# Performance work log

Hardware: AMD Instinct MI355X
Metric: run time of the kernel (lower is better)

The kernel has to match this reference:

```python
import jax, jax.numpy as jnp
import numpy as np

TOP_N = 16

def pairwise_l2(q, c):
    # Euclidean distance via ||q||^2 + ||c||^2 - 2 q.c, matching torch.cdist(p=2)
    qn = jnp.sum(q * q, axis=-1, keepdims=True)        # [B,S,1]
    cn = jnp.sum(c * c, axis=-1)[:, None, :]           # [B,1,C]
    d2 = qn + cn - 2.0 * jnp.einsum('bsd,bcd->bsc', q, c)
    return jnp.sqrt(jnp.maximum(d2, 0.0))

def setup_inputs() -> dict:
    key = jax.random.key(0)
    k1, k2, k3, k4, k5 = jax.random.split(key, 5)
    B, S, C, K, D = 4, 1024, 4096, 64, 256
    return {
        'query_embeddings': jax.random.normal(k1, (B, S, D), jnp.float32),
        'context_embeddings': jax.random.normal(k2, (B, C, D), jnp.float32),
        'memory_embeddings': jax.random.normal(k3, (B, K, D), jnp.float32),
        'W': jax.random.normal(k4, (D, D), jnp.float32) / jnp.sqrt(jnp.float32(D)),
        'b': jax.random.normal(k5, (D,), jnp.float32) * 0.01,
    }

def reference(query_embeddings, context_embeddings, memory_embeddings, W, b):
    # latent_query_projection (nn.Linear): x @ W^T + b
    qp = jnp.einsum('bsd,ed->bse', query_embeddings, W) + b
    d_ctx = pairwise_l2(qp, context_embeddings)                       # [B,S,C]
    mem = memory_embeddings.reshape(memory_embeddings.shape[0], -1,
                                    memory_embeddings.shape[-1])
    d_mem = pairwise_l2(qp, mem)                                      # [B,S,K]
    distances = jnp.concatenate([d_ctx, d_mem], axis=-1)              # [B,S,C+K]
    neg_top, idx = jax.lax.top_k(-distances, TOP_N)                   # smallest distances
    return -neg_top, idx
```

## Files before the change

### kernel.cpp

```cpp
#include <hip/hip_runtime.h>
#include <hip/hip_bf16.h>
#include <cfloat>
#include <cmath>

#define B_ 4
#define S_ 1024
#define C_ 4096
#define K_ 64
#define D_ 256
#define NC 4160
#define TOPN 16
#define CAND2 64

typedef __attribute__((ext_vector_type(8))) short short8;
typedef __attribute__((ext_vector_type(4))) float f32x4;

__global__ __launch_bounds__(256) void proj64_kernel(
    const float* __restrict__ q, const float* __restrict__ W,
    const float* __restrict__ bias, double* __restrict__ qp64,
    __hip_bfloat16* __restrict__ qpb)
{
  __shared__ alignas(16) float As[64][36];
  __shared__ alignas(16) float Ws[64][36];
  const int tid = threadIdx.x;
  const int m0 = blockIdx.x * 64;
  const int n0 = blockIdx.y * 64;
  const int tx = tid & 15;
  const int ty = tid >> 4;
  const int lr = tid >> 3;
  const int lk = (tid & 7) * 4;
  double acc[4][4] = {};
  for (int k0 = 0; k0 < D_; k0 += 32) {
    __syncthreads();
    {
      float4 a0 = *(const float4*)&q[(size_t)(m0 + lr) * D_ + k0 + lk];
      float4 a1 = *(const float4*)&q[(size_t)(m0 + lr + 32) * D_ + k0 + lk];
      *(float4*)&As[lr][lk] = a0;
      *(float4*)&As[lr + 32][lk] = a1;
      float4 w0 = *(const float4*)&W[(size_t)(n0 + lr) * D_ + k0 + lk];
      float4 w1 = *(const float4*)&W[(size_t)(n0 + lr + 32) * D_ + k0 + lk];
      *(float4*)&Ws[lr][lk] = w0;
      *(float4*)&Ws[lr + 32][lk] = w1;
    }
    __syncthreads();
    #pragma unroll
    for (int kk = 0; kk < 32; kk += 4) {
      float4 av[4], wv[4];
      #pragma unroll
      for (int i = 0; i < 4; ++i) av[i] = *(const float4*)&As[ty * 4 + i][kk];
      #pragma unroll
      for (int j = 0; j < 4; ++j) wv[j] = *(const float4*)&Ws[tx + 16 * j][kk];
      #pragma unroll
      for (int i = 0; i < 4; ++i)
        #pragma unroll
        for (int j = 0; j < 4; ++j) {
          acc[i][j] = fma((double)av[i].x, (double)wv[j].x, acc[i][j]);
          acc[i][j] = fma((double)av[i].y, (double)wv[j].y, acc[i][j]);
          acc[i][j] = fma((double)av[i].z, (double)wv[j].z, acc[i][j]);
          acc[i][j] = fma((double)av[i].w, (double)wv[j].w, acc[i][j]);
        }
    }
  }
  #pragma unroll
  for (int i = 0; i < 4; ++i) {
    const int m = m0 + ty * 4 + i;
    #pragma unroll
    for (int j = 0; j < 4; ++j) {
      const int n = n0 + tx + 16 * j;
      const double v = acc[i][j] + (double)bias[n];
      qp64[(size_t)m * D_ + n] = v;
      qpb[(size_t)m * D_ + n] = __float2bfloat16((float)v);
    }
  }
}

__global__ __launch_bounds__(256) void cvt_norm_kernel(
    const float* __restrict__ src, unsigned short* __restrict__ dst,
    float* __restrict__ normp, int log2_rows_per_batch, int dst_row_base, int norm_base)
{
  const int e4 = blockIdx.x * 256 + threadIdx.x;
  const int row = e4 >> 6;
  const int b = row >> log2_rows_per_batch;
  const int r = row & ((1 << log2_rows_per_batch) - 1);
  const int k4 = e4 & 63;
  const float4 v = ((const float4*)src)[e4];
  const int R = dst_row_base + r;
  const int g = R >> 4, l15 = R & 15;
  const int k = k4 * 4;
  const int s = k >> 5, lg = (k & 31) >> 3, i = k & 7;
  unsigned short* d = dst + (size_t)b * (NC * D_) +
                      (size_t)g * 4096 + s * 512 + lg * 128 + l15 * 8 + i;
  ushort4 o;
  __hip_bfloat16 h0 = __float2bfloat16(v.x); o.x = *(unsigned short*)&h0;
  __hip_bfloat16 h1 = __float2bfloat16(v.y); o.y = *(unsigned short*)&h1;
  __hip_bfloat16 h2 = __float2bfloat16(v.z); o.z = *(unsigned short*)&h2;
  __hip_bfloat16 h3 = __float2bfloat16(v.w); o.w = *(unsigned short*)&h3;
  *(ushort4*)d = o;
  float sacc = v.x * v.x + v.y * v.y + v.z * v.z + v.w * v.w;
  #pragma unroll
  for (int off = 32; off > 0; off >>= 1) sacc += __shfl_down(sacc, off);
  if ((threadIdx.x & 63) == 0) normp[b * NC + norm_base + r] = sacc;
}

#define UMIN(a, b) ((a) < (b) ? (a) : (b))
#define UMAX(a, b) ((a) < (b) ? (b) : (a))

#define INSERT_CANDS(ACC, CBASE)                                              \
  {                                                                           \
    const float4 cn4 = *(const float4*)&cnb[(CBASE) + lg * 4];                \
    unsigned k0, k1, k2, k3;                                                  \
    {                                                                         \
      unsigned kk[4];                                                         \
      _Pragma("unroll")                                                       \
      for (int r = 0; r < 4; ++r) {                                           \
        const float d2v = fmaf(-2.0f, (ACC)[r], ((const float*)&cn4)[r]);     \
        kk[r] = (__float_as_uint(d2v) & 0xFFFFE000u)                          \
                | (unsigned)((CBASE) + lg * 4 + r);                           \
      }                                                                       \
      unsigned t;                                                             \
      t = UMIN(kk[0], kk[1]); kk[1] = UMAX(kk[0], kk[1]); kk[0] = t;          \
      t = UMIN(kk[2], kk[3]); kk[3] = UMAX(kk[2], kk[3]); kk[2] = t;          \
      t = UMIN(kk[0], kk[2]); kk[2] = UMAX(kk[0], kk[2]); kk[0] = t;          \
      t = UMIN(kk[1], kk[3]); kk[3] = UMAX(kk[1], kk[3]); kk[1] = t;          \
      t = UMIN(kk[1], kk[2]); kk[2] = UMAX(kk[1], kk[2]); kk[1] = t;          \
      k0 = kk[0]; k1 = kk[1]; k2 = kk[2]; k3 = kk[3];                         \
    }                                                                         \
    unsigned nl[16];                                                          \
    nl[0] = UMIN(ld[0], k0);                                                  \
    nl[1] = UMIN(UMIN(ld[1], UMAX(ld[0], k0)), k1);                           \
    nl[2] = UMIN(UMIN(ld[2], UMAX(ld[1], k0)),                                \
                 UMIN(UMAX(ld[0], k1), k2));                                  \
    nl[3] = UMIN(UMIN(UMIN(ld[3], UMAX(ld[2], k0)),                           \
                      UMIN(UMAX(ld[1], k1), UMAX(ld[0], k2))), k3);           \
    _Pragma("unroll")                                                         \
    for (int i = 4; i < 16; ++i) {                                            \
      nl[i] = UMIN(UMIN(UMIN(ld[i], UMAX(ld[i - 1], k0)),                     \
                        UMIN(UMAX(ld[i - 2], k1), UMAX(ld[i - 3], k2))),      \
                   UMAX(ld[i - 4], k3));                                      \
    }                                                                         \
    _Pragma("unroll")                                                         \
    for (int i = 0; i < 16; ++i) ld[i] = nl[i];                               \
  }

#define MFMA_CHAIN(ACC, FRAGS)                                                \
  f32x4 ACC;                                                                  \
  {                                                                           \
    f32x4 c0_ = {0.f,0.f,0.f,0.f}, c1_ = {0.f,0.f,0.f,0.f};                   \
    f32x4 c2_ = {0.f,0.f,0.f,0.f}, c3_ = {0.f,0.f,0.f,0.f};                   \
    c0_ = __builtin_amdgcn_mfma_f32_16x16x32_bf16((FRAGS)[0], bfr[0], c0_, 0, 0, 0); \
    c1_ = __builtin_amdgcn_mfma_f32_16x16x32_bf16((FRAGS)[1], bfr[1], c1_, 0, 0, 0); \
    c2_ = __builtin_amdgcn_mfma_f32_16x16x32_bf16((FRAGS)[2], bfr[2], c2_, 0, 0, 0); \
    c3_ = __builtin_amdgcn_mfma_f32_16x16x32_bf16((FRAGS)[3], bfr[3], c3_, 0, 0, 0); \
    c0_ = __builtin_amdgcn_mfma_f32_16x16x32_bf16((FRAGS)[4], bfr[4], c0_, 0, 0, 0); \
    c1_ = __builtin_amdgcn_mfma_f32_16x16x32_bf16((FRAGS)[5], bfr[5], c1_, 0, 0, 0); \
    c2_ = __builtin_amdgcn_mfma_f32_16x16x32_bf16((FRAGS)[6], bfr[6], c2_, 0, 0, 0); \
    c3_ = __builtin_amdgcn_mfma_f32_16x16x32_bf16((FRAGS)[7], bfr[7], c3_, 0, 0, 0); \
    ACC = (c0_ + c1_) + (c2_ + c3_);                                          \
  }

__global__ __launch_bounds__(256) void dist_topk_kernel(
    const __hip_bfloat16* __restrict__ qpb, const unsigned short* __restrict__ candb,
    const float* __restrict__ cn, unsigned* __restrict__ topidx)
{
  const int b = blockIdx.x & 3;
  const int split = (blockIdx.x >> 2) & 3;
  const int rt = blockIdx.x >> 4;
  const int row0 = rt * 16;
  const int tid = threadIdx.x;
  const int w = tid >> 6;
  const int lane = tid & 63;
  const int l15 = lane & 15;
  const int lg = lane >> 4;

  __shared__ unsigned md[16][16][17];

  short8 bfr[8];
  {
    const short* qrow = (const short*)qpb + ((size_t)(b * S_ + row0 + l15)) * D_ + lg * 8;
    #pragma unroll
    for (int s = 0; s < 8; ++s) bfr[s] = *(const short8*)(qrow + s * 32);
  }

  const float* cnb = cn + b * NC;
  const short* cbp = (const short*)candb + (size_t)b * NC * D_ + lg * 128 + l15 * 8;

  unsigned ld[16];
  #pragma unroll
  for (int i = 0; i < TOPN; ++i) ld[i] = 0xFFFFFFFFu;

  const int gbase = split + 4 * w;
  const int gtail = 256 + split;

  short8 aA[8], aB[8];
  #pragma unroll
  for (int s = 0; s < 8; ++s)
    aA[s] = *(const short8*)(cbp + (size_t)gbase * 4096 + s * 512);

  for (int j = 0; j < 8; ++j) {
    const int gA = gbase + 32 * j;
    const int gB = gA + 16;
    #pragma unroll
    for (int s = 0; s < 8; ++s)
      aB[s] = *(const short8*)(cbp + (size_t)gB * 4096 + s * 512);

    MFMA_CHAIN(acc, aA);

    if (j < 7) {
      #pragma unroll
      for (int s = 0; s < 8; ++s)
        aA[s] = *(const short8*)(cbp + (size_t)(gA + 32) * 4096 + s * 512);
    } else if (w == 3) {
      #pragma unroll
      for (int s = 0; s < 8; ++s)
        aA[s] = *(const short8*)(cbp + (size_t)gtail * 4096 + s * 512);
    }

    MFMA_CHAIN(acc2, aB);

    INSERT_CANDS(acc, gA * 16);
    INSERT_CANDS(acc2, gB * 16);
  }
  if (w == 3) {
    MFMA_CHAIN(acc, aA);
    INSERT_CANDS(acc, gtail * 16);
  }

  const int lid = w * 4 + lg;
  #pragma unroll
  for (int i = 0; i < TOPN; ++i) md[l15][lid][i] = ld[i];
  __syncthreads();

  {
    const int g = lane >> 4;
    const int h = l15;
    const int row = w * 4 + g;
    int ptr = 0;
    unsigned cur = md[row][h][0];
    unsigned mykey = 0xFFFFFFFFu;
    #pragma unroll
    for (int it = 0; it < TOPN; ++it) {
      unsigned m = cur;
      #pragma unroll
      for (int off = 8; off > 0; off >>= 1) {
        const unsigned o = __shfl_xor(m, off, 16);
        m = (o < m) ? o : m;
      }
      if (h == it) mykey = m;
      if (cur == m) {
        ++ptr;
        cur = (ptr < TOPN) ? md[row][h][ptr] : 0xFFFFFFFFu;
      }
    }
    unsigned* dst = topidx + ((size_t)(b * S_ + row0 + row)) * CAND2 + split * TOPN;
    dst[h] = mykey;
  }
}

__global__ __launch_bounds__(256) void refine_kernel(
    const double* __restrict__ qp64, const float* __restrict__ ctx,
    const float* __restrict__ mem, const unsigned* __restrict__ topidx,
    float* __restrict__ out)
{
  const int row_global = blockIdx.x;
  const int tid = threadIdx.x;
  const int w = tid >> 6;
  const int lane = tid & 63;
  const int c2 = lane >> 5;
  const int ll = lane & 31;
  const int b = row_global >> 10;

  __shared__ int    sel[32];
  __shared__ double d2s[64];
  __shared__ int    ids_s[64];

  if (w == 0) {
    unsigned key = topidx[(size_t)row_global * CAND2 + lane];
    #pragma unroll
    for (int k = 2; k <= 64; k <<= 1) {
      #pragma unroll
      for (int j2 = k >> 1; j2 > 0; j2 >>= 1) {
        const unsigned o = __shfl_xor(key, j2);
        const bool up = ((lane & k) == 0);
        const bool keep_min = (((lane & j2) == 0) == up);
        const bool less = key < o;
        if (keep_min ? !less : less) key = o;
      }
    }
    if (lane < 32) sel[lane] = (int)(key & 0x1FFFu);
  }
  if (w == 1 && lane < 32) { d2s[32 + lane] = DBL_MAX; ids_s[32 + lane] = 0x7fffffff; }
  __syncthreads();

  const double* qrow = qp64 + (size_t)row_global * D_;
  double qd[8];
  #pragma unroll
  for (int t = 0; t < 8; t += 2) {
    double2 v = *(const double2*)&qrow[ll * 8 + t];
    qd[t] = v.x; qd[t + 1] = v.y;
  }

  int cis[4]; float4 cva[4], cvb[4];
  #pragma unroll
  for (int j = 0; j < 4; ++j) cis[j] = sel[w * 8 + 2 * j + c2];
  #pragma unroll
  for (int j = 0; j < 4; ++j) {
    const int ci = cis[j];
    const float* cp = (ci < C_) ? ctx + ((size_t)b * C_ + ci) * D_
                                : mem + ((size_t)b * K_ + (ci - C_)) * D_;
    cva[j] = *(const float4*)&cp[ll * 8];
    cvb[j] = *(const float4*)&cp[ll * 8 + 4];
  }

  #pragma unroll
  for (int j = 0; j < 4; ++j) {
    double a0 = 0.0, a1 = 0.0, df;
    df = qd[0] - (double)cva[j].x; a0 = fma(df, df, a0);
    df = qd[1] - (double)cva[j].y; a1 = fma(df, df, a1);
    df = qd[2] - (double)cva[j].z; a0 = fma(df, df, a0);
    df = qd[3] - (double)cva[j].w; a1 = fma(df, df, a1);
    df = qd[4] - (double)cvb[j].x; a0 = fma(df, df, a0);
    df = qd[5] - (double)cvb[j].y; a1 = fma(df, df, a1);
    df = qd[6] - (double)cvb[j].z; a0 = fma(df, df, a0);
    df = qd[7] - (double)cvb[j].w; a1 = fma(df, df, a1);
    double acc = a0 + a1;
    #pragma unroll
    for (int off = 16; off > 0; off >>= 1) acc += __shfl_down(acc, off, 32);
    if (ll == 0) { d2s[w * 8 + 2 * j + c2] = acc; ids_s[w * 8 + 2 * j + c2] = cis[j]; }
  }
  __syncthreads();

  if (w == 0) {
    double d2 = d2s[lane];
    int    ci = ids_s[lane];
    #pragma unroll
    for (int k = 2; k <= 64; k <<= 1) {
      #pragma unroll
      for (int j2 = k >> 1; j2 > 0; j2 >>= 1) {
        const double od2 = __shfl_xor(d2, j2);
        const int    oci = __shfl_xor(ci, j2);
        const bool up = ((lane & k) == 0);
        const bool less = (d2 < od2) || (d2 == od2 && ci < oci);
        const bool keep_min = (((lane & j2) == 0) == up);
        const bool take = keep_min ? !less : less;
        if (take) { d2 = od2; ci = oci; }
      }
    }
    if (lane < TOPN) {
      const size_t obase = (size_t)row_global * TOPN;
      out[obase + lane] = (float)sqrt(d2 < 0.0 ? 0.0 : d2);
      out[(size_t)B_ * S_ * TOPN + obase + lane] = (float)ci;
    }
  }
}

extern "C" void kernel_launch(void* const* d_in, const int* in_sizes, int n_in,
                              void* d_out, int out_size, void* d_ws, size_t ws_size,
                              hipStream_t stream) {
  const float* q    = (const float*)d_in[0];
  const float* ctx  = (const float*)d_in[1];
  const float* mem  = (const float*)d_in[2];
  const float* W    = (const float*)d_in[3];
  const float* bias = (const float*)d_in[4];
  float* out = (float*)d_out;

  double* qp64 = (double*)d_ws;
  __hip_bfloat16* qpb = (__hip_bfloat16*)(qp64 + (size_t)B_ * S_ * D_);
  unsigned short* candb = (unsigned short*)(qpb + (size_t)B_ * S_ * D_);
  float* cn    = (float*)(candb + (size_t)B_ * NC * D_);
  unsigned* topidx = (unsigned*)(cn + (size_t)B_ * NC);

  proj64_kernel<<<dim3(64, 4), 256, 0, stream>>>(q, W, bias, qp64, qpb);
  cvt_norm_kernel<<<(B_ * C_ * 64) / 256, 256, 0, stream>>>(ctx, candb, cn, 12, 0, 0);
  cvt_norm_kernel<<<(B_ * K_ * 64) / 256, 256, 0, stream>>>(mem, candb, cn, 6, C_, C_);
  dist_topk_kernel<<<1024, 256, 0, stream>>>(qpb, candb, cn, topidx);
  refine_kernel<<<B_ * S_, 256, 0, stream>>>(qp64, ctx, mem, topidx, out);
}
```

Baseline: 91.65 us.

## Merge prep kernels into one launch and split candidate scan eight ways

```diff
diff --git a/kernel.cpp b/kernel.cpp
--- a/kernel.cpp
+++ b/kernel.cpp
@@ -10,86 +10,95 @@
 #define D_ 256
 #define NC 4160
 #define TOPN 16
-#define CAND2 64
+#define NSPLIT 8
+#define CANDK 128
 
 typedef __attribute__((ext_vector_type(8))) short short8;
 typedef __attribute__((ext_vector_type(4))) float f32x4;
 
-__global__ __launch_bounds__(256) void proj64_kernel(
+#define UMIN(a, b) ((a) < (b) ? (a) : (b))
+#define UMAX(a, b) ((a) < (b) ? (b) : (a))
+
+__global__ __launch_bounds__(256) void prep_kernel(
     const float* __restrict__ q, const float* __restrict__ W,
     const float* __restrict__ bias, double* __restrict__ qp64,
-    __hip_bfloat16* __restrict__ qpb)
+    __hip_bfloat16* __restrict__ qpb,
+    const float* __restrict__ ctx, const float* __restrict__ mem,
+    unsigned short* __restrict__ candb, float* __restrict__ cn)
 {
   __shared__ alignas(16) float As[64][36];
   __shared__ alignas(16) float Ws[64][36];
+  const int blk = blockIdx.x;
   const int tid = threadIdx.x;
-  const int m0 = blockIdx.x * 64;
-  const int n0 = blockIdx.y * 64;
-  const int tx = tid & 15;
-  const int ty = tid >> 4;
-  const int lr = tid >> 3;
-  const int lk = (tid & 7) * 4;
-  double acc[4][4] = {};
-  for (int k0 = 0; k0 < D_; k0 += 32) {
-    __syncthreads();
-    {
-      float4 a0 = *(const float4*)&q[(size_t)(m0 + lr) * D_ + k0 + lk];
-      float4 a1 = *(const float4*)&q[(size_t)(m0 + lr + 32) * D_ + k0 + lk];
-      *(float4*)&As[lr][lk] = a0;
-      *(float4*)&As[lr + 32][lk] = a1;
-      float4 w0 = *(const float4*)&W[(size_t)(n0 + lr) * D_ + k0 + lk];
-      float4 w1 = *(const float4*)&W[(size_t)(n0 + lr + 32) * D_ + k0 + lk];
-      *(float4*)&Ws[lr][lk] = w0;
-      *(float4*)&Ws[lr + 32][lk] = w1;
-    }
-    __syncthreads();
-    #pragma unroll
-    for (int kk = 0; kk < 32; kk += 4) {
-      float4 av[4], wv[4];
-      #pragma unroll
-      for (int i = 0; i < 4; ++i) av[i] = *(const float4*)&As[ty * 4 + i][kk];
-      #pragma unroll
-      for (int j = 0; j < 4; ++j) wv[j] = *(const float4*)&Ws[tx + 16 * j][kk];
-      #pragma unroll
-      for (int i = 0; i < 4; ++i)
+
+  if (blk < 256) {
+    const int m0 = (blk & 63) * 64;
+    const int n0 = (blk >> 6) * 64;
+    const int tx = tid & 15;
+    const int ty = tid >> 4;
+    const int lr = tid >> 3;
+    const int lk = (tid & 7) * 4;
+    double acc[4][4] = {};
+    for (int k0 = 0; k0 < D_; k0 += 32) {
+      __syncthreads();
+      {
+        float4 a0 = *(const float4*)&q[(size_t)(m0 + lr) * D_ + k0 + lk];
+        float4 a1 = *(const float4*)&q[(size_t)(m0 + lr + 32) * D_ + k0 + lk];
+        *(float4*)&As[lr][lk] = a0;
+        *(float4*)&As[lr + 32][lk] = a1;
+        float4 w0 = *(const float4*)&W[(size_t)(n0 + lr) * D_ + k0 + lk];
+        float4 w1 = *(const float4*)&W[(size_t)(n0 + lr + 32) * D_ + k0 + lk];
+        *(float4*)&Ws[lr][lk] = w0;
+        *(float4*)&Ws[lr + 32][lk] = w1;
+      }
+      __syncthreads();
+      #pragma unroll
+      for (int kk = 0; kk < 32; kk += 4) {
+        float4 av[4], wv[4];
         #pragma unroll
-        for (int j = 0; j < 4; ++j) {
-          acc[i][j] = fma((double)av[i].x, (double)wv[j].x, acc[i][j]);
-          acc[i][j] = fma((double)av[i].y, (double)wv[j].y, acc[i][j]);
-          acc[i][j] = fma((double)av[i].z, (double)wv[j].z, acc[i][j]);
-          acc[i][j] = fma((double)av[i].w, (double)wv[j].w, acc[i][j]);
-        }
-    }
-  }
-  #pragma unroll
-  for (int i = 0; i < 4; ++i) {
-    const int m = m0 + ty * 4 + i;
-    #pragma unroll
-    for (int j = 0; j < 4; ++j) {
-      const int n = n0 + tx + 16 * j;
-      const double v = acc[i][j] + (double)bias[n];
-      qp64[(size_t)m * D_ + n] = v;
-      qpb[(size_t)m * D_ + n] = __float2bfloat16((float)v);
-    }
-  }
-}
-
-__global__ __launch_bounds__(256) void cvt_norm_kernel(
-    const float* __restrict__ src, unsigned short* __restrict__ dst,
-    float* __restrict__ normp, int log2_rows_per_batch, int dst_row_base, int norm_base)
-{
-  const int e4 = blockIdx.x * 256 + threadIdx.x;
+        for (int i = 0; i < 4; ++i) av[i] = *(const float4*)&As[ty * 4 + i][kk];
+        #pragma unroll
+        for (int j = 0; j < 4; ++j) wv[j] = *(const float4*)&Ws[tx + 16 * j][kk];
+        #pragma unroll
+        for (int i = 0; i < 4; ++i)
+          #pragma unroll
+          for (int j = 0; j < 4; ++j) {
+            acc[i][j] = fma((double)av[i].x, (double)wv[j].x, acc[i][j]);
+            acc[i][j] = fma((double)av[i].y, (double)wv[j].y, acc[i][j]);
+            acc[i][j] = fma((double)av[i].z, (double)wv[j].z, acc[i][j]);
+            acc[i][j] = fma((double)av[i].w, (double)wv[j].w, acc[i][j]);
+          }
+      }
+    }
+    #pragma unroll
+    for (int i = 0; i < 4; ++i) {
+      const int m = m0 + ty * 4 + i;
+      #pragma unroll
+      for (int j = 0; j < 4; ++j) {
+        const int n = n0 + tx + 16 * j;
+        const double v = acc[i][j] + (double)bias[n];
+        qp64[(size_t)m * D_ + n] = v;
+        qpb[(size_t)m * D_ + n] = __float2bfloat16((float)v);
+      }
+    }
+    return;
+  }
+
+  const float* src;
+  int e4, log2rpb, row_base;
+  if (blk < 256 + 4096) { src = ctx; e4 = (blk - 256) * 256 + tid; log2rpb = 12; row_base = 0; }
+  else                  { src = mem; e4 = (blk - 4352) * 256 + tid; log2rpb = 6; row_base = C_; }
   const int row = e4 >> 6;
-  const int b = row >> log2_rows_per_batch;
-  const int r = row & ((1 << log2_rows_per_batch) - 1);
+  const int b = row >> log2rpb;
+  const int r = row & ((1 << log2rpb) - 1);
   const int k4 = e4 & 63;
   const float4 v = ((const float4*)src)[e4];
-  const int R = dst_row_base + r;
+  const int R = row_base + r;
   const int g = R >> 4, l15 = R & 15;
   const int k = k4 * 4;
-  const int s = k >> 5, lg = (k & 31) >> 3, i = k & 7;
-  unsigned short* d = dst + (size_t)b * (NC * D_) +
-                      (size_t)g * 4096 + s * 512 + lg * 128 + l15 * 8 + i;
+  const int s = k >> 5, lg = (k & 31) >> 3, ii = k & 7;
+  unsigned short* d = candb + (size_t)b * (NC * D_) +
+                      (size_t)g * 4096 + s * 512 + lg * 128 + l15 * 8 + ii;
   ushort4 o;
   __hip_bfloat16 h0 = __float2bfloat16(v.x); o.x = *(unsigned short*)&h0;
   __hip_bfloat16 h1 = __float2bfloat16(v.y); o.y = *(unsigned short*)&h1;
@@ -99,11 +108,8 @@
   float sacc = v.x * v.x + v.y * v.y + v.z * v.z + v.w * v.w;
   #pragma unroll
   for (int off = 32; off > 0; off >>= 1) sacc += __shfl_down(sacc, off);
-  if ((threadIdx.x & 63) == 0) normp[b * NC + norm_base + r] = sacc;
+  if ((tid & 63) == 0) cn[b * NC + row_base + r] = sacc;
 }
-
-#define UMIN(a, b) ((a) < (b) ? (a) : (b))
-#define UMAX(a, b) ((a) < (b) ? (b) : (a))
 
 #define INSERT_CANDS(ACC, CBASE)                                              \
   {                                                                           \
@@ -163,8 +169,8 @@
     const float* __restrict__ cn, unsigned* __restrict__ topidx)
 {
   const int b = blockIdx.x & 3;
-  const int split = (blockIdx.x >> 2) & 3;
-  const int rt = blockIdx.x >> 4;
+  const int split = (blockIdx.x >> 2) & 7;
+  const int rt = blockIdx.x >> 5;
   const int row0 = rt * 16;
   const int tid = threadIdx.x;
   const int w = tid >> 6;
@@ -188,28 +194,28 @@
   #pragma unroll
   for (int i = 0; i < TOPN; ++i) ld[i] = 0xFFFFFFFFu;
 
-  const int gbase = split + 4 * w;
+  const bool has_tail = (w == 3 && split < 4);
   const int gtail = 256 + split;
 
   short8 aA[8], aB[8];
   #pragma unroll
   for (int s = 0; s < 8; ++s)
-    aA[s] = *(const short8*)(cbp + (size_t)gbase * 4096 + s * 512);
-
-  for (int j = 0; j < 8; ++j) {
-    const int gA = gbase + 32 * j;
-    const int gB = gA + 16;
+    aA[s] = *(const short8*)(cbp + (size_t)(split + 8 * w) * 4096 + s * 512);
+
+  for (int j = 0; j < 4; ++j) {
+    const int gA = split + 8 * (w + 8 * j);
+    const int gB = gA + 32;
     #pragma unroll
     for (int s = 0; s < 8; ++s)
       aB[s] = *(const short8*)(cbp + (size_t)gB * 4096 + s * 512);
 
     MFMA_CHAIN(acc, aA);
 
-    if (j < 7) {
+    if (j < 3) {
       #pragma unroll
       for (int s = 0; s < 8; ++s)
-        aA[s] = *(const short8*)(cbp + (size_t)(gA + 32) * 4096 + s * 512);
-    } else if (w == 3) {
+        aA[s] = *(const short8*)(cbp + (size_t)(gA + 64) * 4096 + s * 512);
+    } else if (has_tail) {
       #pragma unroll
       for (int s = 0; s < 8; ++s)
         aA[s] = *(const short8*)(cbp + (size_t)gtail * 4096 + s * 512);
@@ -220,7 +226,7 @@
     INSERT_CANDS(acc, gA * 16);
     INSERT_CANDS(acc2, gB * 16);
   }
-  if (w == 3) {
+  if (has_tail) {
     MFMA_CHAIN(acc, aA);
     INSERT_CANDS(acc, gtail * 16);
   }
@@ -251,7 +257,7 @@
         cur = (ptr < TOPN) ? md[row][h][ptr] : 0xFFFFFFFFu;
       }
     }
-    unsigned* dst = topidx + ((size_t)(b * S_ + row0 + row)) * CAND2 + split * TOPN;
+    unsigned* dst = topidx + ((size_t)(b * S_ + row0 + row)) * CANDK + split * TOPN;
     dst[h] = mykey;
   }
 }
@@ -269,12 +275,12 @@
   const int ll = lane & 31;
   const int b = row_global >> 10;
 
-  __shared__ int    sel[32];
+  __shared__ unsigned sA[64], sB[64];
   __shared__ double d2s[64];
   __shared__ int    ids_s[64];
 
-  if (w == 0) {
-    unsigned key = topidx[(size_t)row_global * CAND2 + lane];
+  if (w < 2) {
+    unsigned key = topidx[(size_t)row_global * CANDK + w * 64 + lane];
     #pragma unroll
     for (int k = 2; k <= 64; k <<= 1) {
       #pragma unroll
@@ -286,9 +292,9 @@
         if (keep_min ? !less : less) key = o;
       }
     }
-    if (lane < 32) sel[lane] = (int)(key & 0x1FFFu);
-  }
-  if (w == 1 && lane < 32) { d2s[32 + lane] = DBL_MAX; ids_s[32 + lane] = 0x7fffffff; }
+    if (w == 0) sA[lane] = key; else sB[lane] = key;
+  }
+  if (w == 2 && lane < 32) { d2s[32 + lane] = DBL_MAX; ids_s[32 + lane] = 0x7fffffff; }
   __syncthreads();
 
   const double* qrow = qp64 + (size_t)row_global * D_;
@@ -301,7 +307,11 @@
 
   int cis[4]; float4 cva[4], cvb[4];
   #pragma unroll
-  for (int j = 0; j < 4; ++j) cis[j] = sel[w * 8 + 2 * j + c2];
+  for (int j = 0; j < 4; ++j) {
+    const int p = w * 8 + 2 * j + c2;
+    const unsigned kk = UMIN(sA[p], sB[31 - p]);
+    cis[j] = (int)(kk & 0x1FFFu);
+  }
   #pragma unroll
   for (int j = 0; j < 4; ++j) {
     const int ci = cis[j];
@@ -369,9 +379,7 @@
   float* cn    = (float*)(candb + (size_t)B_ * NC * D_);
   unsigned* topidx = (unsigned*)(cn + (size_t)B_ * NC);
 
-  proj64_kernel<<<dim3(64, 4), 256, 0, stream>>>(q, W, bias, qp64, qpb);
-  cvt_norm_kernel<<<(B_ * C_ * 64) / 256, 256, 0, stream>>>(ctx, candb, cn, 12, 0, 0);
-  cvt_norm_kernel<<<(B_ * K_ * 64) / 256, 256, 0, stream>>>(mem, candb, cn, 6, C_, C_);
-  dist_topk_kernel<<<1024, 256, 0, stream>>>(qpb, candb, cn, topidx);
+  prep_kernel<<<4416, 256, 0, stream>>>(q, W, bias, qp64, qpb, ctx, mem, candb, cn);
+  dist_topk_kernel<<<2048, 256, 0, stream>>>(qpb, candb, cn, topidx);
   refine_kernel<<<B_ * S_, 256, 0, stream>>>(qp64, ctx, mem, topidx, out);
 }
```

Result: faster. 86.32 us (-5.8%).
